# Kernel tuning notes

Measured on AMD Instinct MI355X. Metric: run time of the kernel, lower is better.

Reference implementation:

```python
import jax, jax.numpy as jnp
import numpy as np
import math

B, L, D = 4, 4096, 1024
M = 256  # num random features
EPS = 1e-06


def setup_inputs() -> dict:
    key = jax.random.key(0)
    kq, kk, kv, kp = jax.random.split(key, 4)
    Q = jax.random.normal(kq, (B, L, D), dtype=jnp.float32)
    K = jax.random.normal(kk, (B, L, D), dtype=jnp.float32)
    V = jax.random.normal(kv, (B, L, D), dtype=jnp.float32)
    # Gaussian random projection (ortho_features=False path): shape (num_features, d_model)
    projection = jax.random.normal(kp, (M, D), dtype=jnp.float32)
    return {"Q": Q, "K": K, "V": V, "projection": projection}


def reference(Q, K, V, projection):
    d_model = Q.shape[-1]
    m = projection.shape[0]
    inv_sqrt_d = 1.0 / math.sqrt(d_model)
    # random features: exp((x / sqrt(d)) @ P^T)
    rf_q = jnp.exp(jnp.einsum('bld,md->blm', Q * inv_sqrt_d, projection)) / math.sqrt(m)  # (B,L,M)
    rf_k = jnp.exp(jnp.einsum('bld,md->blm', K * inv_sqrt_d, projection))                 # (B,L,M)
    # linear attention: KV state and normalizer
    KV = jnp.einsum('blm,bld->bmd', rf_k, V)   # (B,M,D)
    Z = jnp.sum(rf_k, axis=1)                   # (B,M)
    out = jnp.einsum('blm,bmd->bld', rf_q, KV)  # (B,L,D)
    normalizer = jnp.einsum('blm,bm->bl', rf_q, Z) + EPS  # (B,L)
    return out / normalizer[..., None]
```

## Files before the change

kernel.cpp:

```cpp
#include <hip/hip_runtime.h>
#include <math.h>

#define NB 4
#define LL 4096
#define DD 1024
#define MM 256

typedef short s16x8 __attribute__((ext_vector_type(8)));
typedef short s16x4 __attribute__((ext_vector_type(4)));
typedef float fx4 __attribute__((ext_vector_type(4)));
typedef unsigned u32x2 __attribute__((ext_vector_type(2)));
typedef unsigned u32x4 __attribute__((ext_vector_type(4)));

__device__ __forceinline__ float b2f(short s) {
  union { unsigned u; float f; } v;
  v.u = ((unsigned)(unsigned short)s) << 16;
  return v.f;
}
__device__ __forceinline__ short f2b(float f) {
  union { float f; unsigned u; } v;
  v.f = f;
  unsigned r = (v.u + 0x7fffu + ((v.u >> 16) & 1u)) >> 16;
  return (short)(unsigned short)r;
}
__device__ __forceinline__ unsigned cvt2(float lo, float hi) {
  unsigned r;
  asm("v_cvt_pk_bf16_f32 %0, %1, %2" : "=v"(r) : "v"(lo), "v"(hi));
  return r;
}
__device__ __forceinline__ int keyf(int m) { return (m ^ (m >> 2)) & 3; }

typedef __attribute__((address_space(1))) const void* gas1_t;
typedef __attribute__((address_space(3))) void* las3_t;
#define GLL16(g, l) __builtin_amdgcn_global_load_lds((gas1_t)(const void*)(g), (las3_t)(void*)(l), 16, 0, 0)

__global__ __launch_bounds__(256) void k_cast(const float* __restrict__ in, short* __restrict__ out, int n4) {
  int i = blockIdx.x * 256 + threadIdx.x;
  if (i >= n4) return;
  float4 v = ((const float4*)in)[i];
  s16x4 s;
  s[0] = f2b(v.x); s[1] = f2b(v.y); s[2] = f2b(v.z); s[3] = f2b(v.w);
  ((s16x4*)out)[i] = s;
}

__global__ __launch_bounds__(256, 2) void k_qk(const float* __restrict__ Q, const float* __restrict__ K,
                                               const short* __restrict__ Pb,
                                               short* __restrict__ rfq, short* __restrict__ rfkT,
                                               float* __restrict__ Zz) {
  __shared__ float As[4][2048];
  __shared__ short Bs[2][8192];
  int z = blockIdx.z, mode = z >> 2, b = z & 3;
  int l0 = blockIdx.x * 64;
  const float* X = mode ? K : Q;
  int tid = threadIdx.x, lane = tid & 63, w = tid >> 6;
  int m16 = lane & 15, kg = lane >> 4;

  int af0 = tid, af1 = tid + 256;
  int ar0 = af0 >> 3, ag0 = af0 & 7, ar1 = af1 >> 3, ag1 = af1 & 7;
  const float* aS0 = X + ((size_t)b * LL + l0 + ar0) * DD + (ag0 ^ (ar0 & 7)) * 4;
  const float* aS1 = X + ((size_t)b * LL + l0 + ar1) * DD + (ag1 ^ (ar1 & 7)) * 4;
  const short* bS[4];
  #pragma unroll
  for (int j = 0; j < 4; ++j) {
    int fl = tid + j * 256, m = fl >> 2, ch = fl & 3;
    bS[j] = Pb + (size_t)m * DD + (ch ^ keyf(m)) * 8;
  }

  fx4 acc[4][4] = {};

  GLL16(aS0, &As[0][af0 * 4]);
  GLL16(aS1, &As[0][af1 * 4]);
  #pragma unroll
  for (int j = 0; j < 4; ++j) GLL16(bS[j], &Bs[0][(tid + j * 256) * 8]);
  GLL16(aS0 + 32, &As[1][af0 * 4]);
  GLL16(aS1 + 32, &As[1][af1 * 4]);
  GLL16(aS0 + 64, &As[2][af0 * 4]);
  GLL16(aS1 + 64, &As[2][af1 * 4]);

  for (int t = 0; t < 32; ++t) {
    int Ab = t & 3, Bb = t & 1;
    if (t < 31) {
      int ko = (t + 1) * 32;
      #pragma unroll
      for (int j = 0; j < 4; ++j) GLL16(bS[j] + ko, &Bs[Bb ^ 1][(tid + j * 256) * 8]);
    }
    if (t < 29) {
      int ko = (t + 3) * 32;
      int An = (t + 3) & 3;
      GLL16(aS0 + ko, &As[An][af0 * 4]);
      GLL16(aS1 + ko, &As[An][af1 * 4]);
    }
    __builtin_amdgcn_sched_barrier(0);
    if (t <= 28)      asm volatile("s_waitcnt vmcnt(8)" ::: "memory");
    else if (t == 29) asm volatile("s_waitcnt vmcnt(6)" ::: "memory");
    else if (t == 30) asm volatile("s_waitcnt vmcnt(4)" ::: "memory");
    else              asm volatile("s_waitcnt vmcnt(0)" ::: "memory");
    __builtin_amdgcn_sched_barrier(0);
    __builtin_amdgcn_s_barrier();
    __builtin_amdgcn_sched_barrier(0);

    s16x8 af[4], bf[4];
    #pragma unroll
    for (int mi = 0; mi < 4; ++mi) {
      int r = mi * 16 + m16, rk = r & 7;
      const float* pr = &As[Ab][r * 32];
      fx4 a0 = *(const fx4*)(pr + ((2 * kg) ^ rk) * 4);
      fx4 a1 = *(const fx4*)(pr + ((2 * kg + 1) ^ rk) * 4);
      u32x4 aw;
      aw[0] = cvt2(a0[0], a0[1]); aw[1] = cvt2(a0[2], a0[3]);
      aw[2] = cvt2(a1[0], a1[1]); aw[3] = cvt2(a1[2], a1[3]);
      af[mi] = *(s16x8*)&aw;
    }
    #pragma unroll
    for (int ni = 0; ni < 4; ++ni) {
      int m = w * 64 + ni * 16 + m16;
      bf[ni] = *(const s16x8*)&Bs[Bb][m * 32 + (kg ^ keyf(m)) * 8];
    }
    #pragma unroll
    for (int mi = 0; mi < 4; ++mi)
      #pragma unroll
      for (int ni = 0; ni < 4; ++ni)
        acc[mi][ni] = __builtin_amdgcn_mfma_f32_16x16x32_bf16(af[mi], bf[ni], acc[mi][ni], 0, 0, 0);

    __builtin_amdgcn_sched_barrier(0);
    __builtin_amdgcn_s_barrier();
    __builtin_amdgcn_sched_barrier(0);
  }

  if (mode == 0) {
    #pragma unroll
    for (int mi = 0; mi < 4; ++mi)
      #pragma unroll
      for (int ni = 0; ni < 4; ++ni) {
        int r0 = mi * 16 + (kg << 2);
        int c = w * 64 + ni * 16 + m16;
        #pragma unroll
        for (int u = 0; u < 4; ++u)
          rfq[((size_t)b * LL + l0 + r0 + u) * MM + c] = f2b(expf(acc[mi][ni][u] * 0.03125f) * 0.0625f);
      }
  } else {
    __syncthreads();
    short* T = (short*)As;
    float zp[4] = {0.f, 0.f, 0.f, 0.f};
    #pragma unroll
    for (int mi = 0; mi < 4; ++mi)
      #pragma unroll
      for (int ni = 0; ni < 4; ++ni) {
        int l = mi * 16 + (kg << 2);
        int m = w * 64 + ni * 16 + m16;
        int key = (m & 7) << 3;
        float e0 = expf(acc[mi][ni][0] * 0.03125f);
        float e1 = expf(acc[mi][ni][1] * 0.03125f);
        float e2 = expf(acc[mi][ni][2] * 0.03125f);
        float e3 = expf(acc[mi][ni][3] * 0.03125f);
        zp[ni] += e0 + e1 + e2 + e3;
        *(unsigned*)&T[m * 64 + (l ^ key)] = cvt2(e0, e1);
        *(unsigned*)&T[m * 64 + ((l ^ key) + 2)] = cvt2(e2, e3);
      }
    #pragma unroll
    for (int ni = 0; ni < 4; ++ni) {
      zp[ni] += __shfl_xor(zp[ni], 16);
      zp[ni] += __shfl_xor(zp[ni], 32);
    }
    if (kg == 0) {
      #pragma unroll
      for (int ni = 0; ni < 4; ++ni)
        atomicAdd(&Zz[b * MM + w * 64 + ni * 16 + m16], zp[ni]);
    }
    __syncthreads();
    int m = tid, mkey = (m & 7) << 3;
    short* dst = rfkT + ((size_t)b * MM + m) * LL + l0;
    #pragma unroll
    for (int j = 0; j < 8; ++j) {
      s16x8 v = *(const s16x8*)&T[m * 64 + ((j * 8) ^ mkey)];
      *(s16x8*)(dst + j * 8) = v;
    }
  }
}

__global__ __launch_bounds__(512) void k_kv(const float* __restrict__ V, const short* __restrict__ rfkT,
                                            float* __restrict__ KVp) {
  __shared__ float Vs[2][32 * 129];
  __shared__ short Ak[2][256 * 32];
  int d0 = blockIdx.x * 128, kc = blockIdx.y, b = blockIdx.z;
  int ls = kc * 512;
  int tid = threadIdx.x, lane = tid & 63, w = tid >> 6;
  int wm = w >> 1, wd = w & 1;
  int m16 = lane & 15, kg = lane >> 4;

  int vl = tid >> 4, vf = (tid & 15) * 8;
  const float* Vb = V + ((size_t)b * LL + ls + vl) * DD + d0 + vf;

  int am = tid >> 2, as = tid & 3;
  int acs = as ^ keyf(am);
  const short* AkS0 = rfkT + ((size_t)b * MM + am) * LL + ls + acs * 8;
  const short* AkS1 = rfkT + ((size_t)b * MM + am + 128) * LL + ls + acs * 8;

  fx4 acc[4][4] = {};
  float4 pv0, pv1;

  pv0 = *(const float4*)(Vb);
  pv1 = *(const float4*)(Vb + 4);
  GLL16(AkS0, &Ak[0][tid * 8]);
  GLL16(AkS1, &Ak[0][(tid + 512) * 8]);
  #pragma unroll
  for (int j = 0; j < 4; ++j) {
    Vs[0][vl * 129 + vf + j] = ((const float*)&pv0)[j];
    Vs[0][vl * 129 + vf + 4 + j] = ((const float*)&pv1)[j];
  }
  __syncthreads();

  for (int ch = 0; ch < 16; ++ch) {
    int cur = ch & 1, nxt = cur ^ 1;
    if (ch < 15) {
      int lo = (ch + 1) * 32;
      pv0 = *(const float4*)(Vb + (size_t)lo * DD);
      pv1 = *(const float4*)(Vb + (size_t)lo * DD + 4);
      GLL16(AkS0 + lo, &Ak[nxt][tid * 8]);
      GLL16(AkS1 + lo, &Ak[nxt][(tid + 512) * 8]);
    }
    s16x8 af[4];
    #pragma unroll
    for (int mi = 0; mi < 4; ++mi) {
      int m = wm * 64 + mi * 16 + m16;
      af[mi] = *(const s16x8*)&Ak[cur][m * 32 + ((kg ^ keyf(m)) * 8)];
    }
    #pragma unroll
    for (int ni = 0; ni < 4; ++ni) {
      int d = wd * 64 + ni * 16 + m16;
      const float* vs = &Vs[cur][kg * 8 * 129 + d];
      u32x4 bw;
      bw[0] = cvt2(vs[0], vs[129]);
      bw[1] = cvt2(vs[258], vs[387]);
      bw[2] = cvt2(vs[516], vs[645]);
      bw[3] = cvt2(vs[774], vs[903]);
      s16x8 bf = *(s16x8*)&bw;
      #pragma unroll
      for (int mi = 0; mi < 4; ++mi)
        acc[mi][ni] = __builtin_amdgcn_mfma_f32_16x16x32_bf16(af[mi], bf, acc[mi][ni], 0, 0, 0);
    }
    if (ch < 15) {
      #pragma unroll
      for (int j = 0; j < 4; ++j) {
        Vs[nxt][vl * 129 + vf + j] = ((const float*)&pv0)[j];
        Vs[nxt][vl * 129 + vf + 4 + j] = ((const float*)&pv1)[j];
      }
    }
    __syncthreads();
  }

  float* dst = KVp + (((size_t)kc * NB + b) * DD + d0) * MM;
  #pragma unroll
  for (int mi = 0; mi < 4; ++mi)
    #pragma unroll
    for (int ni = 0; ni < 4; ++ni) {
      int d = wd * 64 + ni * 16 + m16;
      int m = wm * 64 + mi * 16 + (kg << 2);
      *(float4*)(dst + (size_t)d * MM + m) = *(float4*)&acc[mi][ni];
    }
}

__global__ __launch_bounds__(256) void k_red(const float* __restrict__ KVp, float* __restrict__ KVTf) {
  int i = blockIdx.x * 256 + threadIdx.x;
  const float4* p = (const float4*)KVp;
  float4 s = p[i];
  #pragma unroll
  for (int k = 1; k < 8; ++k) {
    float4 v = p[i + k * 262144];
    s.x += v.x; s.y += v.y; s.z += v.z; s.w += v.w;
  }
  ((float4*)KVTf)[i] = s;
}

__global__ __launch_bounds__(512) void k_out(const short* __restrict__ rfq, const float* __restrict__ KVTf,
                                             const float* __restrict__ Zz, float* __restrict__ out) {
  __shared__ short Aq[2][8192];
  __shared__ short Bv[2][8192];
  __shared__ float zl[256];
  __shared__ float np[512];
  __shared__ float nf[128];
  int l0 = blockIdx.x * 128, d0 = blockIdx.y * 128, b = blockIdx.z;
  int tid = threadIdx.x, lane = tid & 63, w = tid >> 6;
  int wr = w >> 2, wc = w & 3;
  int brow = tid >> 2, bq = (tid & 3) * 16;
  int bkey = (brow & 7) << 3;
  const float* Kf = KVTf + ((size_t)b * DD + d0 + brow) * MM + bq;
  short* Bw0 = &Bv[0][brow * 64 + (bq ^ bkey)];
  short* Bw1 = &Bv[0][brow * 64 + ((bq + 8) ^ bkey)];
  const short* Ab = rfq + ((size_t)b * LL + l0) * MM;
  int f1 = tid + 512;
  int ar0 = tid >> 3, ac0 = tid & 7, ar1 = f1 >> 3, ac1 = f1 & 7;
  int nrow = tid & 127, nsub = tid >> 7;
  if (tid < 256) zl[tid] = Zz[b * MM + tid];
  fx4 acc[4][2] = {};
  float4 pb[4];
  float na = 0.f;

  #pragma unroll
  for (int i = 0; i < 4; ++i) pb[i] = *(const float4*)(Kf + i * 4);
  GLL16(Ab + (size_t)ar0 * MM + (ac0 ^ (ar0 & 7)) * 8, &Aq[0][tid * 8]);
  GLL16(Ab + (size_t)ar1 * MM + (ac1 ^ (ar1 & 7)) * 8, &Aq[0][f1 * 8]);
  {
    u32x2 v0, v1;
    v0[0] = cvt2(pb[0].x, pb[0].y); v0[1] = cvt2(pb[0].z, pb[0].w);
    v1[0] = cvt2(pb[1].x, pb[1].y); v1[1] = cvt2(pb[1].z, pb[1].w);
    *(u32x2*)Bw0 = v0;
    *(u32x2*)(Bw0 + 4) = v1;
    v0[0] = cvt2(pb[2].x, pb[2].y); v0[1] = cvt2(pb[2].z, pb[2].w);
    v1[0] = cvt2(pb[3].x, pb[3].y); v1[1] = cvt2(pb[3].z, pb[3].w);
    *(u32x2*)Bw1 = v0;
    *(u32x2*)(Bw1 + 4) = v1;
  }
  __syncthreads();

  for (int t = 0; t < 4; ++t) {
    int cur = t & 1, nxt = cur ^ 1;
    int m1 = ((t + 1) & 3) * 64;
    #pragma unroll
    for (int i = 0; i < 4; ++i) pb[i] = *(const float4*)(Kf + m1 + i * 4);
    GLL16(Ab + (size_t)ar0 * MM + m1 + (ac0 ^ (ar0 & 7)) * 8, &Aq[nxt][tid * 8]);
    GLL16(Ab + (size_t)ar1 * MM + m1 + (ac1 ^ (ar1 & 7)) * 8, &Aq[nxt][f1 * 8]);
    #pragma unroll
    for (int kk = 0; kk < 16; ++kk) {
      int k = nsub * 16 + kk;
      na += b2f(Aq[cur][nrow * 64 + (k ^ ((nrow & 7) << 3))]) * zl[t * 64 + k];
    }
    #pragma unroll
    for (int ks = 0; ks < 2; ++ks) {
      int kb = ks * 32 + (lane >> 4) * 8;
      s16x8 af[4], bf[2];
      #pragma unroll
      for (int mi = 0; mi < 4; ++mi) {
        int row = wr * 64 + mi * 16 + (lane & 15);
        af[mi] = *(const s16x8*)&Aq[cur][row * 64 + (kb ^ ((row & 7) << 3))];
      }
      #pragma unroll
      for (int ni = 0; ni < 2; ++ni) {
        int row = wc * 32 + ni * 16 + (lane & 15);
        bf[ni] = *(const s16x8*)&Bv[cur][row * 64 + (kb ^ ((row & 7) << 3))];
      }
      #pragma unroll
      for (int mi = 0; mi < 4; ++mi)
        #pragma unroll
        for (int ni = 0; ni < 2; ++ni)
          acc[mi][ni] = __builtin_amdgcn_mfma_f32_16x16x32_bf16(af[mi], bf[ni], acc[mi][ni], 0, 0, 0);
    }
    {
      u32x2 v0, v1;
      v0[0] = cvt2(pb[0].x, pb[0].y); v0[1] = cvt2(pb[0].z, pb[0].w);
      v1[0] = cvt2(pb[1].x, pb[1].y); v1[1] = cvt2(pb[1].z, pb[1].w);
      *(u32x2*)(Bw0 + nxt * 8192) = v0;
      *(u32x2*)(Bw0 + nxt * 8192 + 4) = v1;
      v0[0] = cvt2(pb[2].x, pb[2].y); v0[1] = cvt2(pb[2].z, pb[2].w);
      v1[0] = cvt2(pb[3].x, pb[3].y); v1[1] = cvt2(pb[3].z, pb[3].w);
      *(u32x2*)(Bw1 + nxt * 8192) = v0;
      *(u32x2*)(Bw1 + nxt * 8192 + 4) = v1;
    }
    __syncthreads();
  }
  np[tid] = na;
  __syncthreads();
  if (tid < 128) nf[tid] = np[tid] + np[tid + 128] + np[tid + 256] + np[tid + 384] + 1e-6f;
  __syncthreads();
  #pragma unroll
  for (int mi = 0; mi < 4; ++mi)
    #pragma unroll
    for (int ni = 0; ni < 2; ++ni) {
      int l = wr * 64 + mi * 16 + ((lane >> 4) << 2);
      int d = d0 + wc * 32 + ni * 16 + (lane & 15);
      #pragma unroll
      for (int u = 0; u < 4; ++u)
        out[((size_t)b * LL + l0 + l + u) * DD + d] = acc[mi][ni][u] / nf[l + u];
    }
}

extern "C" void kernel_launch(void* const* d_in, const int* in_sizes, int n_in,
                              void* d_out, int out_size, void* d_ws, size_t ws_size,
                              hipStream_t stream) {
  const float* Q = (const float*)d_in[0];
  const float* K = (const float*)d_in[1];
  const float* V = (const float*)d_in[2];
  const float* P = (const float*)d_in[3];
  float* out = (float*)d_out;
  char* ws = (char*)d_ws;

  short* Pb   = (short*)(ws + 0);
  float* Zz   = (float*)(ws + 524288);
  float* KVTf = (float*)(ws + 528384);
  short* rfq  = (short*)(ws + 4722688);
  short* rfkT = (short*)(ws + 13111296);
  float* KVp  = (float*)(ws + 21499904);

  k_cast<<<256, 256, 0, stream>>>(P, Pb, 65536);
  (void)hipMemsetAsync(Zz, 0, 4096, stream);
  k_qk<<<dim3(64, 1, 2 * NB), 256, 0, stream>>>(Q, K, Pb, rfq, rfkT, Zz);
  k_kv<<<dim3(8, 8, NB), 512, 0, stream>>>(V, rfkT, KVp);
  k_red<<<1024, 256, 0, stream>>>(KVp, KVTf);
  k_out<<<dim3(32, 8, NB), 512, 0, stream>>>(rfq, KVTf, Zz, out);
}
```

Measured before the change: 141.8 us.

## Double threads per block in k_qk and halve k_kv d-tile for more parallelism

```diff
diff --git a/kernel.cpp b/kernel.cpp
--- a/kernel.cpp
+++ b/kernel.cpp
@@ -43,7 +43,7 @@
   ((s16x4*)out)[i] = s;
 }
 
-__global__ __launch_bounds__(256, 2) void k_qk(const float* __restrict__ Q, const float* __restrict__ K,
+__global__ __launch_bounds__(512, 4) void k_qk(const float* __restrict__ Q, const float* __restrict__ K,
                                                const short* __restrict__ Pb,
                                                short* __restrict__ rfq, short* __restrict__ rfkT,
                                                float* __restrict__ Zz) {
@@ -53,56 +53,48 @@
   int l0 = blockIdx.x * 64;
   const float* X = mode ? K : Q;
   int tid = threadIdx.x, lane = tid & 63, w = tid >> 6;
+  int wr = w >> 2, wc = w & 3;
   int m16 = lane & 15, kg = lane >> 4;
 
-  int af0 = tid, af1 = tid + 256;
-  int ar0 = af0 >> 3, ag0 = af0 & 7, ar1 = af1 >> 3, ag1 = af1 & 7;
-  const float* aS0 = X + ((size_t)b * LL + l0 + ar0) * DD + (ag0 ^ (ar0 & 7)) * 4;
-  const float* aS1 = X + ((size_t)b * LL + l0 + ar1) * DD + (ag1 ^ (ar1 & 7)) * 4;
-  const short* bS[4];
-  #pragma unroll
-  for (int j = 0; j < 4; ++j) {
-    int fl = tid + j * 256, m = fl >> 2, ch = fl & 3;
-    bS[j] = Pb + (size_t)m * DD + (ch ^ keyf(m)) * 8;
-  }
-
-  fx4 acc[4][4] = {};
-
-  GLL16(aS0, &As[0][af0 * 4]);
-  GLL16(aS1, &As[0][af1 * 4]);
-  #pragma unroll
-  for (int j = 0; j < 4; ++j) GLL16(bS[j], &Bs[0][(tid + j * 256) * 8]);
-  GLL16(aS0 + 32, &As[1][af0 * 4]);
-  GLL16(aS1 + 32, &As[1][af1 * 4]);
-  GLL16(aS0 + 64, &As[2][af0 * 4]);
-  GLL16(aS1 + 64, &As[2][af1 * 4]);
+  int arow = tid >> 3, ag = tid & 7;
+  const float* aS = X + ((size_t)b * LL + l0 + arow) * DD + (ag ^ (arow & 7)) * 4;
+  int bm0 = tid >> 2, bc0 = tid & 3;
+  const short* bS0 = Pb + (size_t)bm0 * DD + (bc0 ^ keyf(bm0)) * 8;
+  const short* bS1 = Pb + (size_t)(bm0 + 128) * DD + (bc0 ^ keyf(bm0 + 128)) * 8;
+
+  fx4 acc[2][4] = {};
+
+  GLL16(aS, &As[0][tid * 4]);
+  GLL16(bS0, &Bs[0][tid * 8]);
+  GLL16(bS1, &Bs[0][(tid + 512) * 8]);
+  GLL16(aS + 32, &As[1][tid * 4]);
+  GLL16(aS + 64, &As[2][tid * 4]);
 
   for (int t = 0; t < 32; ++t) {
     int Ab = t & 3, Bb = t & 1;
     if (t < 31) {
       int ko = (t + 1) * 32;
-      #pragma unroll
-      for (int j = 0; j < 4; ++j) GLL16(bS[j] + ko, &Bs[Bb ^ 1][(tid + j * 256) * 8]);
+      GLL16(bS0 + ko, &Bs[Bb ^ 1][tid * 8]);
+      GLL16(bS1 + ko, &Bs[Bb ^ 1][(tid + 512) * 8]);
     }
     if (t < 29) {
       int ko = (t + 3) * 32;
-      int An = (t + 3) & 3;
-      GLL16(aS0 + ko, &As[An][af0 * 4]);
-      GLL16(aS1 + ko, &As[An][af1 * 4]);
-    }
-    __builtin_amdgcn_sched_barrier(0);
-    if (t <= 28)      asm volatile("s_waitcnt vmcnt(8)" ::: "memory");
-    else if (t == 29) asm volatile("s_waitcnt vmcnt(6)" ::: "memory");
-    else if (t == 30) asm volatile("s_waitcnt vmcnt(4)" ::: "memory");
+      GLL16(aS + ko, &As[(t + 3) & 3][tid * 4]);
+    }
+    __builtin_amdgcn_sched_barrier(0);
+    if (t == 0)       asm volatile("s_waitcnt vmcnt(5)" ::: "memory");
+    else if (t <= 28) asm volatile("s_waitcnt vmcnt(4)" ::: "memory");
+    else if (t == 29) asm volatile("s_waitcnt vmcnt(3)" ::: "memory");
+    else if (t == 30) asm volatile("s_waitcnt vmcnt(2)" ::: "memory");
     else              asm volatile("s_waitcnt vmcnt(0)" ::: "memory");
     __builtin_amdgcn_sched_barrier(0);
     __builtin_amdgcn_s_barrier();
     __builtin_amdgcn_sched_barrier(0);
 
-    s16x8 af[4], bf[4];
-    #pragma unroll
-    for (int mi = 0; mi < 4; ++mi) {
-      int r = mi * 16 + m16, rk = r & 7;
+    s16x8 af[2], bf[4];
+    #pragma unroll
+    for (int mi = 0; mi < 2; ++mi) {
+      int r = wr * 32 + mi * 16 + m16, rk = r & 7;
       const float* pr = &As[Ab][r * 32];
       fx4 a0 = *(const fx4*)(pr + ((2 * kg) ^ rk) * 4);
       fx4 a1 = *(const fx4*)(pr + ((2 * kg + 1) ^ rk) * 4);
@@ -113,11 +105,11 @@
     }
     #pragma unroll
     for (int ni = 0; ni < 4; ++ni) {
-      int m = w * 64 + ni * 16 + m16;
+      int m = wc * 64 + ni * 16 + m16;
       bf[ni] = *(const s16x8*)&Bs[Bb][m * 32 + (kg ^ keyf(m)) * 8];
     }
     #pragma unroll
-    for (int mi = 0; mi < 4; ++mi)
+    for (int mi = 0; mi < 2; ++mi)
       #pragma unroll
       for (int ni = 0; ni < 4; ++ni)
         acc[mi][ni] = __builtin_amdgcn_mfma_f32_16x16x32_bf16(af[mi], bf[ni], acc[mi][ni], 0, 0, 0);
@@ -129,11 +121,11 @@
 
   if (mode == 0) {
     #pragma unroll
-    for (int mi = 0; mi < 4; ++mi)
+    for (int mi = 0; mi < 2; ++mi)
       #pragma unroll
       for (int ni = 0; ni < 4; ++ni) {
-        int r0 = mi * 16 + (kg << 2);
-        int c = w * 64 + ni * 16 + m16;
+        int r0 = wr * 32 + mi * 16 + (kg << 2);
+        int c = wc * 64 + ni * 16 + m16;
         #pragma unroll
         for (int u = 0; u < 4; ++u)
           rfq[((size_t)b * LL + l0 + r0 + u) * MM + c] = f2b(expf(acc[mi][ni][u] * 0.03125f) * 0.0625f);
@@ -143,11 +135,11 @@
     short* T = (short*)As;
     float zp[4] = {0.f, 0.f, 0.f, 0.f};
     #pragma unroll
-    for (int mi = 0; mi < 4; ++mi)
+    for (int mi = 0; mi < 2; ++mi)
       #pragma unroll
       for (int ni = 0; ni < 4; ++ni) {
-        int l = mi * 16 + (kg << 2);
-        int m = w * 64 + ni * 16 + m16;
+        int l = wr * 32 + mi * 16 + (kg << 2);
+        int m = wc * 64 + ni * 16 + m16;
         int key = (m & 7) << 3;
         float e0 = expf(acc[mi][ni][0] * 0.03125f);
         float e1 = expf(acc[mi][ni][1] * 0.03125f);
@@ -165,57 +157,53 @@
     if (kg == 0) {
       #pragma unroll
       for (int ni = 0; ni < 4; ++ni)
-        atomicAdd(&Zz[b * MM + w * 64 + ni * 16 + m16], zp[ni]);
+        atomicAdd(&Zz[b * MM + wc * 64 + ni * 16 + m16], zp[ni]);
     }
     __syncthreads();
-    int m = tid, mkey = (m & 7) << 3;
-    short* dst = rfkT + ((size_t)b * MM + m) * LL + l0;
-    #pragma unroll
-    for (int j = 0; j < 8; ++j) {
-      s16x8 v = *(const s16x8*)&T[m * 64 + ((j * 8) ^ mkey)];
+    int m = tid >> 1, half = (tid & 1) * 32;
+    int mkey = (m & 7) << 3;
+    short* dst = rfkT + ((size_t)b * MM + m) * LL + l0 + half;
+    #pragma unroll
+    for (int j = 0; j < 4; ++j) {
+      int l = half + j * 8;
+      s16x8 v = *(const s16x8*)&T[m * 64 + (l ^ mkey)];
       *(s16x8*)(dst + j * 8) = v;
     }
   }
 }
 
-__global__ __launch_bounds__(512) void k_kv(const float* __restrict__ V, const short* __restrict__ rfkT,
-                                            float* __restrict__ KVp) {
-  __shared__ float Vs[2][32 * 129];
+__global__ __launch_bounds__(512, 4) void k_kv(const float* __restrict__ V, const short* __restrict__ rfkT,
+                                               float* __restrict__ KVp) {
+  __shared__ float Vs[2][32 * 65];
   __shared__ short Ak[2][256 * 32];
-  int d0 = blockIdx.x * 128, kc = blockIdx.y, b = blockIdx.z;
+  int d0 = blockIdx.x * 64, kc = blockIdx.y, b = blockIdx.z;
   int ls = kc * 512;
   int tid = threadIdx.x, lane = tid & 63, w = tid >> 6;
   int wm = w >> 1, wd = w & 1;
   int m16 = lane & 15, kg = lane >> 4;
 
-  int vl = tid >> 4, vf = (tid & 15) * 8;
+  int vl = tid >> 4, vf = (tid & 15) * 4;
   const float* Vb = V + ((size_t)b * LL + ls + vl) * DD + d0 + vf;
 
   int am = tid >> 2, as = tid & 3;
-  int acs = as ^ keyf(am);
-  const short* AkS0 = rfkT + ((size_t)b * MM + am) * LL + ls + acs * 8;
-  const short* AkS1 = rfkT + ((size_t)b * MM + am + 128) * LL + ls + acs * 8;
-
-  fx4 acc[4][4] = {};
-  float4 pv0, pv1;
-
-  pv0 = *(const float4*)(Vb);
-  pv1 = *(const float4*)(Vb + 4);
+  const short* AkS0 = rfkT + ((size_t)b * MM + am) * LL + ls + (as ^ keyf(am)) * 8;
+  const short* AkS1 = rfkT + ((size_t)b * MM + am + 128) * LL + ls + (as ^ keyf(am + 128)) * 8;
+
+  fx4 acc[4][2] = {};
+  float4 pv;
+
+  pv = *(const float4*)(Vb);
   GLL16(AkS0, &Ak[0][tid * 8]);
   GLL16(AkS1, &Ak[0][(tid + 512) * 8]);
   #pragma unroll
-  for (int j = 0; j < 4; ++j) {
-    Vs[0][vl * 129 + vf + j] = ((const float*)&pv0)[j];
-    Vs[0][vl * 129 + vf + 4 + j] = ((const float*)&pv1)[j];
-  }
+  for (int j = 0; j < 4; ++j) Vs[0][vl * 65 + vf + j] = ((const float*)&pv)[j];
   __syncthreads();
 
   for (int ch = 0; ch < 16; ++ch) {
     int cur = ch & 1, nxt = cur ^ 1;
     if (ch < 15) {
       int lo = (ch + 1) * 32;
-      pv0 = *(const float4*)(Vb + (size_t)lo * DD);
-      pv1 = *(const float4*)(Vb + (size_t)lo * DD + 4);
+      pv = *(const float4*)(Vb + (size_t)lo * DD);
       GLL16(AkS0 + lo, &Ak[nxt][tid * 8]);
       GLL16(AkS1 + lo, &Ak[nxt][(tid + 512) * 8]);
     }
@@ -226,14 +214,14 @@
       af[mi] = *(const s16x8*)&Ak[cur][m * 32 + ((kg ^ keyf(m)) * 8)];
     }
     #pragma unroll
-    for (int ni = 0; ni < 4; ++ni) {
-      int d = wd * 64 + ni * 16 + m16;
-      const float* vs = &Vs[cur][kg * 8 * 129 + d];
+    for (int ni = 0; ni < 2; ++ni) {
+      int d = wd * 32 + ni * 16 + m16;
+      const float* vs = &Vs[cur][kg * 8 * 65 + d];
       u32x4 bw;
-      bw[0] = cvt2(vs[0], vs[129]);
-      bw[1] = cvt2(vs[258], vs[387]);
-      bw[2] = cvt2(vs[516], vs[645]);
-      bw[3] = cvt2(vs[774], vs[903]);
+      bw[0] = cvt2(vs[0], vs[65]);
+      bw[1] = cvt2(vs[130], vs[195]);
+      bw[2] = cvt2(vs[260], vs[325]);
+      bw[3] = cvt2(vs[390], vs[455]);
       s16x8 bf = *(s16x8*)&bw;
       #pragma unroll
       for (int mi = 0; mi < 4; ++mi)
@@ -241,10 +229,7 @@
     }
     if (ch < 15) {
       #pragma unroll
-      for (int j = 0; j < 4; ++j) {
-        Vs[nxt][vl * 129 + vf + j] = ((const float*)&pv0)[j];
-        Vs[nxt][vl * 129 + vf + 4 + j] = ((const float*)&pv1)[j];
-      }
+      for (int j = 0; j < 4; ++j) Vs[nxt][vl * 65 + vf + j] = ((const float*)&pv)[j];
     }
     __syncthreads();
   }
@@ -253,8 +238,8 @@
   #pragma unroll
   for (int mi = 0; mi < 4; ++mi)
     #pragma unroll
-    for (int ni = 0; ni < 4; ++ni) {
-      int d = wd * 64 + ni * 16 + m16;
+    for (int ni = 0; ni < 2; ++ni) {
+      int d = wd * 32 + ni * 16 + m16;
       int m = wm * 64 + mi * 16 + (kg << 2);
       *(float4*)(dst + (size_t)d * MM + m) = *(float4*)&acc[mi][ni];
     }
@@ -393,8 +378,8 @@
 
   k_cast<<<256, 256, 0, stream>>>(P, Pb, 65536);
   (void)hipMemsetAsync(Zz, 0, 4096, stream);
-  k_qk<<<dim3(64, 1, 2 * NB), 256, 0, stream>>>(Q, K, Pb, rfq, rfkT, Zz);
-  k_kv<<<dim3(8, 8, NB), 512, 0, stream>>>(V, rfkT, KVp);
+  k_qk<<<dim3(64, 1, 2 * NB), 512, 0, stream>>>(Q, K, Pb, rfq, rfkT, Zz);
+  k_kv<<<dim3(16, 8, NB), 512, 0, stream>>>(V, rfkT, KVp);
   k_red<<<1024, 256, 0, stream>>>(KVp, KVTf);
   k_out<<<dim3(32, 8, NB), 512, 0, stream>>>(rfq, KVTf, Zz, out);
 }
```

Measured after the change: 142.4 us. No clear change (+0.4%).
